# Optimization experiments

Hardware: AMD Instinct MI355X
Metric: run time of the kernel (lower is better)

## Reference

```python
import jax, jax.numpy as jnp
import numpy as np

B = 32768
D = 1024          # input_dim
SEL = 512         # select_dim (per-expert selected features)
E = 6             # num_experts
K = 3             # top_k
SH = 32           # shared_dim
INNER = 64        # cross-attn inner dim (4 heads * 16)
HID = 128         # expert hidden


def setup_inputs() -> dict:
    key = jax.random.key(0)
    ks = jax.random.split(key, 16)
    s = lambda i, shape, scale=0.02: (jax.random.normal(ks[i], shape, jnp.float32) * scale)
    return {
        "x": jax.random.normal(ks[0], (B, D), jnp.float32),
        # CrossAttention(query_dim=512, context_dim=512, heads=4, dim_head=16)
        "Wq": s(1, (512, INNER)),
        "Wk": s(2, (512, INNER)),
        "Wv": s(3, (512, INNER)),
        "Wo": s(4, (INNER, 512)),
        "bo": jnp.zeros((512,), jnp.float32),
        # shared_proj: Linear(512, 32)
        "Wsp": s(5, (512, SH)),
        "bsp": jnp.zeros((SH,), jnp.float32),
        # gate: Linear(1024, 6)
        "Wg": s(6, (D, E)),
        "bg": jnp.zeros((E,), jnp.float32),
        # per-expert feature-mask logits
        "mask_logits": jax.random.normal(ks[7], (E, D), jnp.float32),
        # expert MLPs: Linear(544,128) -> ReLU -> Linear(128,1), stacked over experts
        "W1": s(8, (E, SEL + SH, HID)),
        "b1": jnp.zeros((E, HID), jnp.float32),
        "W2": s(9, (E, HID, 1)),
        "b2": jnp.zeros((E, 1), jnp.float32),
    }


def _moe_forward(x, Wq, Wk, Wv, Wo, bo, Wsp, bsp, Wg, bg, mask_logits, W1, b1, W2, b2):
    x_sem = x[:, :512]
    x_vis = x[:, 512:]

    # CrossAttention with a single query token attending to a single context
    # token: softmax over one key is identically 1, so attn output == v.
    v = x_vis @ Wv                      # [B, INNER]
    shared_token = v @ Wo + bo          # to_out Linear, [B, 512]
    shared_info = shared_token @ Wsp + bsp  # [B, SH]

    # Gating: top-k experts per sample, softmax over selected logits
    gate_logits = x @ Wg + bg                       # [B, E]
    topk_scores, topk_idx = jax.lax.top_k(gate_logits, K)  # [B, K]
    topk_w = jax.nn.softmax(topk_scores, axis=1)    # [B, K]

    # Per-expert learned feature selection (top-512 of sigmoid(mask_logits));
    # sigmoid is monotonic but kept for faithfulness.
    mask_prob = jax.nn.sigmoid(mask_logits)         # [E, D]
    _, sel_idx = jax.lax.top_k(mask_prob, SEL)      # [E, SEL]

    # Dense expert evaluation (every expert on every sample), then gather the
    # routed outputs -- same math as the original scatter loop.
    x_sel = jnp.take(x, sel_idx, axis=1)            # [B, E, SEL]
    h = jnp.einsum('bes,esh->beh', x_sel, W1[:, :SEL, :])
    h = h + jnp.einsum('bd,edh->beh', shared_info, W1[:, SEL:, :])
    h = jax.nn.relu(h + b1[None])                   # [B, E, HID]
    expert_out = jnp.einsum('beh,eh->be', h, W2[:, :, 0]) + b2[None, :, 0]  # [B, E]

    routed = jnp.take_along_axis(expert_out, topk_idx, axis=1)  # [B, K]
    return jnp.sum(topk_w * routed, axis=1, keepdims=True)      # [B, 1]


def reference(x, Wq, Wk, Wv, Wo, bo, Wsp, bsp, Wg, bg, mask_logits, W1, b1, W2, b2):
    return _moe_forward(x, Wq, Wk, Wv, Wo, bo, Wsp, bsp, Wg, bg, mask_logits, W1, b1, W2, b2)
```

## Files before the change

### kernel.cpp

```cpp
#include <hip/hip_runtime.h>

#define B 32768
#define D 1024
#define SEL 512
#define E 6
#define K 3
#define SH 32
#define HID 128
#define NKT 16

typedef __attribute__((ext_vector_type(8))) short bf16x8;
typedef __attribute__((ext_vector_type(4))) float f32x4;

__device__ __forceinline__ unsigned short f2bf(float f) {
  unsigned u = __float_as_uint(f);
  return (unsigned short)((u + 0x7fffu + ((u >> 16) & 1u)) >> 16);
}
__device__ __forceinline__ float bf2f(unsigned short h) {
  return __uint_as_float((unsigned)h << 16);
}

__device__ __forceinline__ void gload_lds16(const void* g, void* l) {
  __builtin_amdgcn_global_load_lds(
      (const __attribute__((address_space(1))) void*)g,
      (__attribute__((address_space(3))) void*)l, 16, 0, 0);
}

__global__ void k_sel(const float* __restrict__ ml, int* __restrict__ inv,
                      int* __restrict__ cnt) {
  __shared__ float row[D];
  const int e = blockIdx.x, t = threadIdx.x;
  if (t == 0) cnt[e] = 0;
  row[t] = ml[e * D + t];
  __syncthreads();
  const float v = row[t];
  int rank = 0;
  for (int i = 0; i < D; ++i) {
    float u = row[i];
    rank += (u > v) || (u == v && i < t);
  }
  inv[e * D + t] = (rank < SEL) ? rank : -1;
}

__global__ __launch_bounds__(256) void k_wowsp(
    const float* __restrict__ Wo, const float* __restrict__ Wsp,
    const float* __restrict__ bo, const float* __restrict__ bsp,
    const float* __restrict__ Wg,
    float* __restrict__ WoWsp, float* __restrict__ bfull,
    unsigned short* __restrict__ WgS) {
  __shared__ float red[256];
  const int t = threadIdx.x;
  const int j = t & 31, chunk = t >> 5;
  const int blk = blockIdx.x;
  if (blk < 64) {
    const int i = blk;
    float p = 0.f;
    for (int c = chunk * 64; c < chunk * 64 + 64; ++c)
      p += Wo[i * 512 + c] * Wsp[c * SH + j];
    red[t] = p;
    __syncthreads();
    if (t < 32) {
      float s = 0.f;
      #pragma unroll
      for (int k = 0; k < 8; ++k) s += red[k * 32 + j];
      WoWsp[i * SH + j] = s;
    }
  } else if (blk == 64) {
    float p = 0.f;
    for (int c = chunk * 64; c < chunk * 64 + 64; ++c)
      p += bo[c] * Wsp[c * SH + j];
    red[t] = p;
    __syncthreads();
    if (t < 32) {
      float s = bsp[j];
      #pragma unroll
      for (int k = 0; k < 8; ++k) s += red[k * 32 + j];
      bfull[j] = s;
    }
  } else {
    const int idx = (blk - 65) * 256 + t;
    const int col = idx >> 10, k = idx & 1023;
    float wv = (col < E) ? Wg[(size_t)k * E + col] : 0.f;
    unsigned short hi = f2bf(wv);
    unsigned short lo = f2bf(wv - bf2f(hi));
    WgS[col * D + k] = hi;
    WgS[16 * D + col * D + k] = lo;
  }
}

__global__ __launch_bounds__(256) void k_wfull2(
    const float* __restrict__ Wv, const float* __restrict__ WoWsp,
    float* __restrict__ Wfull) {
  __shared__ float wsh[64 * SH];
  const int t = threadIdx.x;
  for (int idx = t; idx < 64 * SH; idx += 256) wsh[idx] = WoWsp[idx];
  __syncthreads();
  const int c = blockIdx.x * 8 + (t >> 5), j = t & 31;
  float p = 0.f;
  #pragma unroll 8
  for (int i = 0; i < 64; ++i) p += Wv[c * 64 + i] * wsh[i * SH + j];
  Wfull[c * SH + j] = p;
}

__global__ __launch_bounds__(256) void k_w1c(
    const float* __restrict__ W1, const float* __restrict__ b1,
    const int* __restrict__ inv, const float* __restrict__ Wfull,
    const float* __restrict__ bfull,
    unsigned short* __restrict__ W1eT, float* __restrict__ b1c) {
  __shared__ float w1b[SH];
  __shared__ float bf[SH];
  const int e = blockIdx.x >> 7, h = blockIdx.x & 127;
  const int t = threadIdx.x;
  const float* We = W1 + (size_t)e * (SEL + SH) * HID;
  if (t < SH) { w1b[t] = We[(size_t)(SEL + t) * HID + h]; bf[t] = bfull[t]; }
  __syncthreads();
  const int* iv = inv + e * D;
  unsigned short* dst = W1eT + ((size_t)e * HID + h) * D;
  #pragma unroll
  for (int it = 0; it < 4; ++it) {
    int d = t + it * 256;
    int s = iv[d];
    float v = (s >= 0) ? We[(size_t)s * HID + h] : 0.f;
    if (d >= 512) {
      const float* wf = Wfull + (size_t)(d - 512) * SH;
      float p = 0.f;
      #pragma unroll
      for (int j = 0; j < SH; ++j) p += wf[j] * w1b[j];
      v += p;
    }
    dst[d] = f2bf(v);
  }
  if (t == 0) {
    float p = b1[e * HID + h];
    for (int j = 0; j < SH; ++j) p += bf[j] * w1b[j];
    b1c[e * HID + h] = p;
  }
}

template<bool WRITE_XBF>
__global__ __launch_bounds__(256) void k_xgate(
    const float* __restrict__ x, const unsigned short* __restrict__ WgS,
    const float* __restrict__ Wg, const float* __restrict__ bg,
    unsigned short* __restrict__ xbf,
    int* __restrict__ cnt, int* __restrict__ clist, float* __restrict__ wlist) {
  __shared__ __align__(16) char ldsAh[64 * 128];
  __shared__ __align__(16) char ldsAl[64 * 128];
  __shared__ __align__(16) char ldsW[4096];
  __shared__ float gl_s[64][8];
  const int t = threadIdx.x;
  const int bm = blockIdx.x;
  const int w = t >> 6, lane = t & 63;
  const int g = lane >> 4, j = lane & 15;
  const int swz = ((lane & 7) * 16) ^ ((lane >> 3) << 4);

  const char* srcW = (const char*)WgS +
                     (size_t)(w * 8 + (lane >> 3)) * (D * 2) + swz;

  f32x4 acc = {0.f, 0.f, 0.f, 0.f};

  for (int kt = 0; kt < NKT; ++kt) {
    if (kt) __syncthreads();
    gload_lds16(srcW + kt * 128, ldsW + w * 1024);
    #pragma unroll
    for (int it = 0; it < 4; ++it) {
      int r = (t >> 4) + it * 16;
      const float4 v =
          *(const float4*)(x + (size_t)(bm * 64 + r) * D + kt * 64 + (t & 15) * 4);
      ushort4 hh, ll;
      hh.x = f2bf(v.x); hh.y = f2bf(v.y); hh.z = f2bf(v.z); hh.w = f2bf(v.w);
      ll.x = f2bf(v.x - bf2f(hh.x)); ll.y = f2bf(v.y - bf2f(hh.y));
      ll.z = f2bf(v.z - bf2f(hh.z)); ll.w = f2bf(v.w - bf2f(hh.w));
      if (WRITE_XBF)
        *(ushort4*)(xbf + (size_t)(bm * 64 + r) * D + kt * 64 + (t & 15) * 4) = hh;
      const int ao = r * 128 + (((t & 15) * 8) ^ ((r & 7) << 4));
      *(ushort4*)(ldsAh + ao) = hh;
      *(ushort4*)(ldsAl + ao) = ll;
    }
    __syncthreads();
    #pragma unroll
    for (int kk = 0; kk < 2; ++kk) {
      const int kb = kk * 64 + g * 16;
      const int wo = kb ^ ((j & 7) << 4);
      bf16x8 bh = *(const bf16x8*)(ldsW + j * 128 + wo);
      bf16x8 bl = *(const bf16x8*)(ldsW + 2048 + j * 128 + wo);
      const int row = w * 16 + j;
      const int aoff = row * 128 + (kb ^ ((row & 7) << 4));
      bf16x8 ah = *(const bf16x8*)(ldsAh + aoff);
      bf16x8 al = *(const bf16x8*)(ldsAl + aoff);
      acc = __builtin_amdgcn_mfma_f32_16x16x32_bf16(ah, bh, acc, 0, 0, 0);
      acc = __builtin_amdgcn_mfma_f32_16x16x32_bf16(ah, bl, acc, 0, 0, 0);
      acc = __builtin_amdgcn_mfma_f32_16x16x32_bf16(al, bh, acc, 0, 0, 0);
      acc = __builtin_amdgcn_mfma_f32_16x16x32_bf16(al, bl, acc, 0, 0, 0);
    }
  }
  if (j < E) {
    #pragma unroll
    for (int ri = 0; ri < 4; ++ri)
      gl_s[w * 16 + g * 4 + ri][j] = acc[ri];
  }
  __syncthreads();
  if (t < 64) {
    const int tok = bm * 64 + t;
    float gv[E];
    #pragma unroll
    for (int e2 = 0; e2 < E; ++e2) gv[e2] = gl_s[t][e2] + bg[e2];

    float s4[4];
    {
      bool used[E] = {};
      #pragma unroll
      for (int k = 0; k < 4; ++k) {
        float best = -1e30f; int bi = 0;
        for (int e2 = 0; e2 < E; ++e2)
          if (!used[e2] && gv[e2] > best) { best = gv[e2]; bi = e2; }
        used[bi] = true; s4[k] = best;
      }
    }
    unsigned long long flags = __ballot(s4[2] - s4[3] < 4e-3f);
    while (flags) {
      const int fl = __ffsll((long long)flags) - 1;
      flags &= flags - 1;
      const int tokf = bm * 64 + fl;
      float ex[E] = {};
      for (int i = 0; i < 16; ++i) {
        const int d = t + 64 * i;
        float xv = x[(size_t)tokf * D + d];
        const float* wr = Wg + (size_t)d * E;
        #pragma unroll
        for (int e2 = 0; e2 < E; ++e2) ex[e2] += xv * wr[e2];
      }
      #pragma unroll
      for (int e2 = 0; e2 < E; ++e2) {
        float s = ex[e2];
        s += __shfl_xor(s, 1); s += __shfl_xor(s, 2); s += __shfl_xor(s, 4);
        s += __shfl_xor(s, 8); s += __shfl_xor(s, 16); s += __shfl_xor(s, 32);
        ex[e2] = s;
      }
      if (t == fl) {
        #pragma unroll
        for (int e2 = 0; e2 < E; ++e2) gv[e2] = ex[e2] + bg[e2];
      }
    }
    int idx[K]; float sc[K];
    bool used[E] = {};
    #pragma unroll
    for (int k = 0; k < K; ++k) {
      float best = -1e30f; int bi = 0;
      for (int e2 = 0; e2 < E; ++e2)
        if (!used[e2] && gv[e2] > best) { best = gv[e2]; bi = e2; }
      used[bi] = true; sc[k] = best; idx[k] = bi;
    }
    float s1 = __expf(sc[1] - sc[0]), s2 = __expf(sc[2] - sc[0]);
    float inv_s = 1.f / (1.f + s1 + s2);
    float tw[K] = {inv_s, s1 * inv_s, s2 * inv_s};
    const unsigned long long below = (1ULL << t) - 1ULL;
    #pragma unroll
    for (int e2 = 0; e2 < E; ++e2) {
      int myk = -1;
      #pragma unroll
      for (int k = 0; k < K; ++k) if (idx[k] == e2) myk = k;
      unsigned long long m = __ballot(myk >= 0);
      if (m) {
        int tot = __popcll(m);
        int leader = __ffsll((long long)m) - 1;
        int base = 0;
        if (t == leader) base = atomicAdd(&cnt[e2], tot);
        base = __shfl(base, leader);
        if (myk >= 0) {
          int pos = base + __popcll(m & below);
          clist[e2 * B + pos] = (tok << 2) | myk;
          wlist[e2 * B + pos] = tw[myk];
        }
      }
    }
  }
}

template<int AMODE>
__global__ __launch_bounds__(256) void k_gemm(
    const float* __restrict__ x, const unsigned short* __restrict__ xbf,
    const unsigned short* __restrict__ W1eT,
    const int* __restrict__ cnt, const int* __restrict__ clist,
    const float* __restrict__ wlist,
    const float* __restrict__ b1c, const float* __restrict__ W2,
    const float* __restrict__ b2, float* __restrict__ eo4) {
  __shared__ __align__(16) char ldsA[128 * 128];
  __shared__ __align__(16) char ldsB[128 * 128];
  __shared__ int tokl[128];
  __shared__ float red[128];

  const int t = threadIdx.x;
  const int e = blockIdx.x >> 8;
  const int bm = blockIdx.x & 255;
  const int n = cnt[e];
  if (bm * 128 >= n) return;
  const int cb = e * B;

  if (t < 128) {
    int gr = bm * 128 + t;
    tokl[t] = clist[cb + (gr < n ? gr : 0)] >> 2;
  }
  __syncthreads();

  const int w = t >> 6, lane = t & 63;
  const int g = lane >> 4, j = lane & 15;
  const int swz = ((lane & 7) * 16) ^ ((lane >> 3) << 4);

  const char* srcB[4];
  #pragma unroll
  for (int q = 0; q < 4; ++q)
    srcB[q] = (const char*)W1eT +
              (size_t)(e * HID + w * 32 + q * 8 + (lane >> 3)) * (D * 2) + swz;
  const char* srcA[4];
  if (AMODE == 0) {
    #pragma unroll
    for (int q = 0; q < 4; ++q)
      srcA[q] = (const char*)xbf +
                (size_t)tokl[w * 32 + q * 8 + (lane >> 3)] * 2048 + swz;
  }

  f32x4 acc[2][8] = {};

  for (int kt = 0; kt < NKT; ++kt) {
    if (kt) __syncthreads();
    if (AMODE == 0) {
      #pragma unroll
      for (int q = 0; q < 4; ++q)
        gload_lds16(srcA[q] + kt * 128, ldsA + w * 4096 + q * 1024);
    }
    #pragma unroll
    for (int q = 0; q < 4; ++q)
      gload_lds16(srcB[q] + kt * 128, ldsB + w * 4096 + q * 1024);
    if (AMODE == 1) {
      #pragma unroll
      for (int it = 0; it < 8; ++it) {
        int r = (t >> 4) + it * 16;
        const float4 v =
            *(const float4*)(x + (size_t)tokl[r] * D + kt * 64 + (t & 15) * 4);
        ushort4 h4;
        h4.x = f2bf(v.x); h4.y = f2bf(v.y); h4.z = f2bf(v.z); h4.w = f2bf(v.w);
        *(ushort4*)(ldsA + r * 128 + (((t & 15) * 8) ^ ((r & 7) << 4))) = h4;
      }
    }
    __syncthreads();
    #pragma unroll
    for (int kk = 0; kk < 2; ++kk) {
      const int kb = kk * 64 + g * 16;
      bf16x8 aF[2];
      #pragma unroll
      for (int fm = 0; fm < 2; ++fm) {
        int row = w * 32 + fm * 16 + j;
        aF[fm] = *(const bf16x8*)(ldsA + row * 128 + (kb ^ ((row & 7) << 4)));
      }
      #pragma unroll
      for (int fn = 0; fn < 8; ++fn) {
        int col = fn * 16 + j;
        bf16x8 bF = *(const bf16x8*)(ldsB + col * 128 + (kb ^ ((col & 7) << 4)));
        acc[0][fn] = __builtin_amdgcn_mfma_f32_16x16x32_bf16(aF[0], bF, acc[0][fn], 0, 0, 0);
        acc[1][fn] = __builtin_amdgcn_mfma_f32_16x16x32_bf16(aF[1], bF, acc[1][fn], 0, 0, 0);
      }
    }
  }

  float vb1[8], vw2[8];
  #pragma unroll
  for (int fn = 0; fn < 8; ++fn) {
    int col = fn * 16 + j;
    vb1[fn] = b1c[e * HID + col];
    vw2[fn] = W2[e * HID + col];
  }
  #pragma unroll
  for (int fm = 0; fm < 2; ++fm) {
    #pragma unroll
    for (int r = 0; r < 4; ++r) {
      float s = 0.f;
      #pragma unroll
      for (int fn = 0; fn < 8; ++fn)
        s += fmaxf(acc[fm][fn][r] + vb1[fn], 0.f) * vw2[fn];
      s += __shfl_xor(s, 1); s += __shfl_xor(s, 2);
      s += __shfl_xor(s, 4); s += __shfl_xor(s, 8);
      if (j == 0) red[w * 32 + fm * 16 + g * 4 + r] = s;
    }
  }
  __syncthreads();
  if (t < 128) {
    int gr = bm * 128 + t;
    if (gr < n) {
      int en = clist[cb + gr];
      eo4[(size_t)(en >> 2) * 4 + (en & 3)] = wlist[cb + gr] * (red[t] + b2[e]);
    }
  }
}

__global__ void k_comb2(const float* __restrict__ eo4, float* __restrict__ out) {
  const int tok = blockIdx.x * 256 + threadIdx.x;
  float4 v = *(const float4*)(eo4 + (size_t)tok * 4);
  out[tok] = v.x + v.y + v.z;
}

extern "C" void kernel_launch(void* const* d_in, const int* in_sizes, int n_in,
                              void* d_out, int out_size, void* d_ws, size_t ws_size,
                              hipStream_t stream) {
  const float* x   = (const float*)d_in[0];
  const float* Wv  = (const float*)d_in[3];
  const float* Wo  = (const float*)d_in[4];
  const float* bo  = (const float*)d_in[5];
  const float* Wsp = (const float*)d_in[6];
  const float* bsp = (const float*)d_in[7];
  const float* Wg  = (const float*)d_in[8];
  const float* bg  = (const float*)d_in[9];
  const float* ml  = (const float*)d_in[10];
  const float* W1  = (const float*)d_in[11];
  const float* b1  = (const float*)d_in[12];
  const float* W2  = (const float*)d_in[13];
  const float* b2  = (const float*)d_in[14];
  float* out = (float*)d_out;

  char* ws = (char*)d_ws;
  int*   inv   = (int*)ws;
  float* WoWsp = (float*)(ws + 32768);
  float* Wfull = (float*)(ws + 49152);
  float* bfull = (float*)(ws + 114688);
  float* b1c   = (float*)(ws + 118784);
  int*   cnt   = (int*)(ws + 126976);
  unsigned short* WgS = (unsigned short*)(ws + 131072);
  int*   clist = (int*)(ws + 262144);
  float* wlist = (float*)(ws + 1048576);
  float* eo4   = (float*)(ws + 1835008);
  unsigned short* W1eT = (unsigned short*)(ws + 2359296);
  unsigned short* xbf  = (unsigned short*)(ws + 3932160);
  const bool use_xbf = ws_size >= (size_t)3932160 + (size_t)B * D * 2;

  k_sel<<<E, D, 0, stream>>>(ml, inv, cnt);
  k_wowsp<<<129, 256, 0, stream>>>(Wo, Wsp, bo, bsp, Wg, WoWsp, bfull, WgS);
  k_wfull2<<<64, 256, 0, stream>>>(Wv, WoWsp, Wfull);
  k_w1c<<<E * HID, 256, 0, stream>>>(W1, b1, inv, Wfull, bfull, W1eT, b1c);
  if (use_xbf)
    k_xgate<true><<<B / 64, 256, 0, stream>>>(x, WgS, Wg, bg, xbf, cnt, clist, wlist);
  else
    k_xgate<false><<<B / 64, 256, 0, stream>>>(x, WgS, Wg, bg, xbf, cnt, clist, wlist);
  if (use_xbf)
    k_gemm<0><<<E * 256, 256, 0, stream>>>(x, xbf, W1eT, cnt, clist, wlist, b1c, W2, b2, eo4);
  else
    k_gemm<1><<<E * 256, 256, 0, stream>>>(x, xbf, W1eT, cnt, clist, wlist, b1c, W2, b2, eo4);
  k_comb2<<<B / 256, 256, 0, stream>>>(eo4, out);
}
```

Baseline: 175.7 us.

## Split gate GEMM K across waves and drop per-tile block barriers

```diff
diff --git a/kernel.cpp b/kernel.cpp
--- a/kernel.cpp
+++ b/kernel.cpp
@@ -143,67 +143,79 @@
     const float* __restrict__ Wg, const float* __restrict__ bg,
     unsigned short* __restrict__ xbf,
     int* __restrict__ cnt, int* __restrict__ clist, float* __restrict__ wlist) {
-  __shared__ __align__(16) char ldsAh[64 * 128];
-  __shared__ __align__(16) char ldsAl[64 * 128];
-  __shared__ __align__(16) char ldsW[4096];
-  __shared__ float gl_s[64][8];
+  __shared__ __align__(16) char ldsAh[4][32 * 128];
+  __shared__ __align__(16) char ldsAl[4][32 * 128];
+  __shared__ float gl_s[4][32][8];
   const int t = threadIdx.x;
   const int bm = blockIdx.x;
-  const int w = t >> 6, lane = t & 63;
-  const int g = lane >> 4, j = lane & 15;
-  const int swz = ((lane & 7) * 16) ^ ((lane >> 3) << 4);
-
-  const char* srcW = (const char*)WgS +
-                     (size_t)(w * 8 + (lane >> 3)) * (D * 2) + swz;
-
-  f32x4 acc = {0.f, 0.f, 0.f, 0.f};
-
-  for (int kt = 0; kt < NKT; ++kt) {
-    if (kt) __syncthreads();
-    gload_lds16(srcW + kt * 128, ldsW + w * 1024);
-    #pragma unroll
-    for (int it = 0; it < 4; ++it) {
-      int r = (t >> 4) + it * 16;
-      const float4 v =
-          *(const float4*)(x + (size_t)(bm * 64 + r) * D + kt * 64 + (t & 15) * 4);
+  const int w = t >> 6, l = t & 63;
+  const int g = l >> 4, j = l & 15;
+  const int tok0 = bm * 32;
+  const int k0 = w * 256;
+
+  char* Ah = ldsAh[w];
+  char* Al = ldsAl[w];
+
+  f32x4 acc0 = {0.f, 0.f, 0.f, 0.f};
+  f32x4 acc1 = {0.f, 0.f, 0.f, 0.f};
+
+  #pragma unroll
+  for (int tile = 0; tile < 4; ++tile) {
+    const int kb = k0 + tile * 64;
+    #pragma unroll
+    for (int i = 0; i < 8; ++i) {
+      const int r = (l >> 4) + i * 4;
+      const int c = l & 15;
+      float4 v = *(const float4*)(x + (size_t)(tok0 + r) * D + kb + c * 4);
       ushort4 hh, ll;
       hh.x = f2bf(v.x); hh.y = f2bf(v.y); hh.z = f2bf(v.z); hh.w = f2bf(v.w);
       ll.x = f2bf(v.x - bf2f(hh.x)); ll.y = f2bf(v.y - bf2f(hh.y));
       ll.z = f2bf(v.z - bf2f(hh.z)); ll.w = f2bf(v.w - bf2f(hh.w));
       if (WRITE_XBF)
-        *(ushort4*)(xbf + (size_t)(bm * 64 + r) * D + kt * 64 + (t & 15) * 4) = hh;
-      const int ao = r * 128 + (((t & 15) * 8) ^ ((r & 7) << 4));
-      *(ushort4*)(ldsAh + ao) = hh;
-      *(ushort4*)(ldsAl + ao) = ll;
-    }
-    __syncthreads();
+        *(ushort4*)(xbf + (size_t)(tok0 + r) * D + kb + c * 4) = hh;
+      const int ao = r * 128 + ((c * 8) ^ ((r & 7) << 4));
+      *(ushort4*)(Ah + ao) = hh;
+      *(ushort4*)(Al + ao) = ll;
+    }
     #pragma unroll
     for (int kk = 0; kk < 2; ++kk) {
-      const int kb = kk * 64 + g * 16;
-      const int wo = kb ^ ((j & 7) << 4);
-      bf16x8 bh = *(const bf16x8*)(ldsW + j * 128 + wo);
-      bf16x8 bl = *(const bf16x8*)(ldsW + 2048 + j * 128 + wo);
-      const int row = w * 16 + j;
-      const int aoff = row * 128 + (kb ^ ((row & 7) << 4));
-      bf16x8 ah = *(const bf16x8*)(ldsAh + aoff);
-      bf16x8 al = *(const bf16x8*)(ldsAl + aoff);
-      acc = __builtin_amdgcn_mfma_f32_16x16x32_bf16(ah, bh, acc, 0, 0, 0);
-      acc = __builtin_amdgcn_mfma_f32_16x16x32_bf16(ah, bl, acc, 0, 0, 0);
-      acc = __builtin_amdgcn_mfma_f32_16x16x32_bf16(al, bh, acc, 0, 0, 0);
-      acc = __builtin_amdgcn_mfma_f32_16x16x32_bf16(al, bl, acc, 0, 0, 0);
+      bf16x8 bh = *(const bf16x8*)(WgS + (size_t)j * D + kb + kk * 32 + g * 8);
+      bf16x8 bl = *(const bf16x8*)(WgS + (size_t)(16 + j) * D + kb + kk * 32 + g * 8);
+      #pragma unroll
+      for (int rf = 0; rf < 2; ++rf) {
+        const int row = rf * 16 + j;
+        const int aoff = row * 128 + ((kk * 64 + g * 16) ^ ((row & 7) << 4));
+        bf16x8 ah = *(const bf16x8*)(Ah + aoff);
+        bf16x8 al = *(const bf16x8*)(Al + aoff);
+        if (rf == 0) {
+          acc0 = __builtin_amdgcn_mfma_f32_16x16x32_bf16(ah, bh, acc0, 0, 0, 0);
+          acc0 = __builtin_amdgcn_mfma_f32_16x16x32_bf16(ah, bl, acc0, 0, 0, 0);
+          acc0 = __builtin_amdgcn_mfma_f32_16x16x32_bf16(al, bh, acc0, 0, 0, 0);
+          acc0 = __builtin_amdgcn_mfma_f32_16x16x32_bf16(al, bl, acc0, 0, 0, 0);
+        } else {
+          acc1 = __builtin_amdgcn_mfma_f32_16x16x32_bf16(ah, bh, acc1, 0, 0, 0);
+          acc1 = __builtin_amdgcn_mfma_f32_16x16x32_bf16(ah, bl, acc1, 0, 0, 0);
+          acc1 = __builtin_amdgcn_mfma_f32_16x16x32_bf16(al, bh, acc1, 0, 0, 0);
+          acc1 = __builtin_amdgcn_mfma_f32_16x16x32_bf16(al, bl, acc1, 0, 0, 0);
+        }
+      }
     }
   }
   if (j < E) {
     #pragma unroll
-    for (int ri = 0; ri < 4; ++ri)
-      gl_s[w * 16 + g * 4 + ri][j] = acc[ri];
-  }
-  __syncthreads();
-  if (t < 64) {
-    const int tok = bm * 64 + t;
+    for (int ri = 0; ri < 4; ++ri) {
+      gl_s[w][g * 4 + ri][j] = acc0[ri];
+      gl_s[w][16 + g * 4 + ri][j] = acc1[ri];
+    }
+  }
+  __syncthreads();
+  if (t < 32) {
+    const int tok = tok0 + t;
     float gv[E];
     #pragma unroll
-    for (int e2 = 0; e2 < E; ++e2) gv[e2] = gl_s[t][e2] + bg[e2];
+    for (int e2 = 0; e2 < E; ++e2)
+      gv[e2] = gl_s[0][t][e2] + gl_s[1][t][e2] + gl_s[2][t][e2] +
+               gl_s[3][t][e2] + bg[e2];
 
     float s4[4];
     {
@@ -220,10 +232,10 @@
     while (flags) {
       const int fl = __ffsll((long long)flags) - 1;
       flags &= flags - 1;
-      const int tokf = bm * 64 + fl;
+      const int tokf = tok0 + fl;
       float ex[E] = {};
-      for (int i = 0; i < 16; ++i) {
-        const int d = t + 64 * i;
+      for (int i = 0; i < 32; ++i) {
+        const int d = t + 32 * i;
         float xv = x[(size_t)tokf * D + d];
         const float* wr = Wg + (size_t)d * E;
         #pragma unroll
@@ -233,7 +245,7 @@
       for (int e2 = 0; e2 < E; ++e2) {
         float s = ex[e2];
         s += __shfl_xor(s, 1); s += __shfl_xor(s, 2); s += __shfl_xor(s, 4);
-        s += __shfl_xor(s, 8); s += __shfl_xor(s, 16); s += __shfl_xor(s, 32);
+        s += __shfl_xor(s, 8); s += __shfl_xor(s, 16);
         ex[e2] = s;
       }
       if (t == fl) {
@@ -436,9 +448,9 @@
   k_wfull2<<<64, 256, 0, stream>>>(Wv, WoWsp, Wfull);
   k_w1c<<<E * HID, 256, 0, stream>>>(W1, b1, inv, Wfull, bfull, W1eT, b1c);
   if (use_xbf)
-    k_xgate<true><<<B / 64, 256, 0, stream>>>(x, WgS, Wg, bg, xbf, cnt, clist, wlist);
+    k_xgate<true><<<B / 32, 256, 0, stream>>>(x, WgS, Wg, bg, xbf, cnt, clist, wlist);
   else
-    k_xgate<false><<<B / 64, 256, 0, stream>>>(x, WgS, Wg, bg, xbf, cnt, clist, wlist);
+    k_xgate<false><<<B / 32, 256, 0, stream>>>(x, WgS, Wg, bg, xbf, cnt, clist, wlist);
   if (use_xbf)
     k_gemm<0><<<E * 256, 256, 0, stream>>>(x, xbf, W1eT, cnt, clist, wlist, b1c, W2, b2, eo4);
   else
```

Measured after the change: 214.5 us. 1.22x slower.

## Shrink gate kernel tile to 16 tokens and split bf16 MFMA terms across waves

Applied to the files above, without the earlier changes.

```diff
diff --git a/kernel.cpp b/kernel.cpp
--- a/kernel.cpp
+++ b/kernel.cpp
@@ -143,15 +143,17 @@
     const float* __restrict__ Wg, const float* __restrict__ bg,
     unsigned short* __restrict__ xbf,
     int* __restrict__ cnt, int* __restrict__ clist, float* __restrict__ wlist) {
-  __shared__ __align__(16) char ldsAh[64 * 128];
-  __shared__ __align__(16) char ldsAl[64 * 128];
+  __shared__ __align__(16) char ldsAh[16 * 128];
+  __shared__ __align__(16) char ldsAl[16 * 128];
   __shared__ __align__(16) char ldsW[4096];
-  __shared__ float gl_s[64][8];
+  __shared__ float gl_s[4][16][8];
   const int t = threadIdx.x;
   const int bm = blockIdx.x;
   const int w = t >> 6, lane = t & 63;
   const int g = lane >> 4, j = lane & 15;
+  const int tok0 = bm * 16;
   const int swz = ((lane & 7) * 16) ^ ((lane >> 3) << 4);
+  const int r0 = t >> 4, c = t & 15;
 
   const char* srcW = (const char*)WgS +
                      (size_t)(w * 8 + (lane >> 3)) * (D * 2) + swz;
@@ -159,20 +161,17 @@
   f32x4 acc = {0.f, 0.f, 0.f, 0.f};
 
   for (int kt = 0; kt < NKT; ++kt) {
-    if (kt) __syncthreads();
     gload_lds16(srcW + kt * 128, ldsW + w * 1024);
-    #pragma unroll
-    for (int it = 0; it < 4; ++it) {
-      int r = (t >> 4) + it * 16;
+    {
       const float4 v =
-          *(const float4*)(x + (size_t)(bm * 64 + r) * D + kt * 64 + (t & 15) * 4);
+          *(const float4*)(x + (size_t)(tok0 + r0) * D + kt * 64 + c * 4);
       ushort4 hh, ll;
       hh.x = f2bf(v.x); hh.y = f2bf(v.y); hh.z = f2bf(v.z); hh.w = f2bf(v.w);
       ll.x = f2bf(v.x - bf2f(hh.x)); ll.y = f2bf(v.y - bf2f(hh.y));
       ll.z = f2bf(v.z - bf2f(hh.z)); ll.w = f2bf(v.w - bf2f(hh.w));
       if (WRITE_XBF)
-        *(ushort4*)(xbf + (size_t)(bm * 64 + r) * D + kt * 64 + (t & 15) * 4) = hh;
-      const int ao = r * 128 + (((t & 15) * 8) ^ ((r & 7) << 4));
+        *(ushort4*)(xbf + (size_t)(tok0 + r0) * D + kt * 64 + c * 4) = hh;
+      const int ao = r0 * 128 + ((c * 8) ^ ((r0 & 7) << 4));
       *(ushort4*)(ldsAh + ao) = hh;
       *(ushort4*)(ldsAl + ao) = ll;
     }
@@ -181,29 +180,38 @@
     for (int kk = 0; kk < 2; ++kk) {
       const int kb = kk * 64 + g * 16;
       const int wo = kb ^ ((j & 7) << 4);
-      bf16x8 bh = *(const bf16x8*)(ldsW + j * 128 + wo);
-      bf16x8 bl = *(const bf16x8*)(ldsW + 2048 + j * 128 + wo);
-      const int row = w * 16 + j;
-      const int aoff = row * 128 + (kb ^ ((row & 7) << 4));
-      bf16x8 ah = *(const bf16x8*)(ldsAh + aoff);
-      bf16x8 al = *(const bf16x8*)(ldsAl + aoff);
-      acc = __builtin_amdgcn_mfma_f32_16x16x32_bf16(ah, bh, acc, 0, 0, 0);
-      acc = __builtin_amdgcn_mfma_f32_16x16x32_bf16(ah, bl, acc, 0, 0, 0);
-      acc = __builtin_amdgcn_mfma_f32_16x16x32_bf16(al, bh, acc, 0, 0, 0);
-      acc = __builtin_amdgcn_mfma_f32_16x16x32_bf16(al, bl, acc, 0, 0, 0);
-    }
+      const int aoff = j * 128 + (kb ^ ((j & 7) << 4));
+      bf16x8 aF, bF;
+      if (w == 0) {
+        aF = *(const bf16x8*)(ldsAh + aoff);
+        bF = *(const bf16x8*)(ldsW + j * 128 + wo);
+      } else if (w == 1) {
+        aF = *(const bf16x8*)(ldsAl + aoff);
+        bF = *(const bf16x8*)(ldsW + 2048 + j * 128 + wo);
+      } else if (w == 2) {
+        aF = *(const bf16x8*)(ldsAh + aoff);
+        bF = *(const bf16x8*)(ldsW + 2048 + j * 128 + wo);
+      } else {
+        aF = *(const bf16x8*)(ldsAl + aoff);
+        bF = *(const bf16x8*)(ldsW + j * 128 + wo);
+      }
+      acc = __builtin_amdgcn_mfma_f32_16x16x32_bf16(aF, bF, acc, 0, 0, 0);
+    }
+    __syncthreads();
   }
   if (j < E) {
     #pragma unroll
     for (int ri = 0; ri < 4; ++ri)
-      gl_s[w * 16 + g * 4 + ri][j] = acc[ri];
-  }
-  __syncthreads();
-  if (t < 64) {
-    const int tok = bm * 64 + t;
+      gl_s[w][g * 4 + ri][j] = acc[ri];
+  }
+  __syncthreads();
+  if (t < 16) {
+    const int tok = tok0 + t;
     float gv[E];
     #pragma unroll
-    for (int e2 = 0; e2 < E; ++e2) gv[e2] = gl_s[t][e2] + bg[e2];
+    for (int e2 = 0; e2 < E; ++e2)
+      gv[e2] = gl_s[0][t][e2] + gl_s[1][t][e2] + gl_s[2][t][e2] +
+               gl_s[3][t][e2] + bg[e2];
 
     float s4[4];
     {
@@ -220,10 +228,10 @@
     while (flags) {
       const int fl = __ffsll((long long)flags) - 1;
       flags &= flags - 1;
-      const int tokf = bm * 64 + fl;
+      const int tokf = tok0 + fl;
       float ex[E] = {};
-      for (int i = 0; i < 16; ++i) {
-        const int d = t + 64 * i;
+      for (int i = 0; i < 64; ++i) {
+        const int d = t + 16 * i;
         float xv = x[(size_t)tokf * D + d];
         const float* wr = Wg + (size_t)d * E;
         #pragma unroll
@@ -232,8 +240,8 @@
       #pragma unroll
       for (int e2 = 0; e2 < E; ++e2) {
         float s = ex[e2];
-        s += __shfl_xor(s, 1); s += __shfl_xor(s, 2); s += __shfl_xor(s, 4);
-        s += __shfl_xor(s, 8); s += __shfl_xor(s, 16); s += __shfl_xor(s, 32);
+        s += __shfl_xor(s, 1); s += __shfl_xor(s, 2);
+        s += __shfl_xor(s, 4); s += __shfl_xor(s, 8);
         ex[e2] = s;
       }
       if (t == fl) {
@@ -436,9 +444,9 @@
   k_wfull2<<<64, 256, 0, stream>>>(Wv, WoWsp, Wfull);
   k_w1c<<<E * HID, 256, 0, stream>>>(W1, b1, inv, Wfull, bfull, W1eT, b1c);
   if (use_xbf)
-    k_xgate<true><<<B / 64, 256, 0, stream>>>(x, WgS, Wg, bg, xbf, cnt, clist, wlist);
+    k_xgate<true><<<B / 16, 256, 0, stream>>>(x, WgS, Wg, bg, xbf, cnt, clist, wlist);
   else
-    k_xgate<false><<<B / 64, 256, 0, stream>>>(x, WgS, Wg, bg, xbf, cnt, clist, wlist);
+    k_xgate<false><<<B / 16, 256, 0, stream>>>(x, WgS, Wg, bg, xbf, cnt, clist, wlist);
   if (use_xbf)
     k_gemm<0><<<E * 256, 256, 0, stream>>>(x, xbf, W1eT, cnt, clist, wlist, b1c, W2, b2, eo4);
   else
```

Result: slower. 282.8 us (+60.9%).

## Split gate GEMM over K into 4 blocks and move top-k to separate kernel

Applied to the files above, without the earlier changes.

```diff
diff --git a/kernel.cpp b/kernel.cpp
--- a/kernel.cpp
+++ b/kernel.cpp
@@ -140,17 +140,16 @@
 template<bool WRITE_XBF>
 __global__ __launch_bounds__(256) void k_xgate(
     const float* __restrict__ x, const unsigned short* __restrict__ WgS,
-    const float* __restrict__ Wg, const float* __restrict__ bg,
-    unsigned short* __restrict__ xbf,
-    int* __restrict__ cnt, int* __restrict__ clist, float* __restrict__ wlist) {
+    unsigned short* __restrict__ xbf, float* __restrict__ gpart) {
   __shared__ __align__(16) char ldsAh[64 * 128];
   __shared__ __align__(16) char ldsAl[64 * 128];
   __shared__ __align__(16) char ldsW[4096];
-  __shared__ float gl_s[64][8];
   const int t = threadIdx.x;
-  const int bm = blockIdx.x;
+  const int bm = blockIdx.x >> 2;
+  const int ks = blockIdx.x & 3;
   const int w = t >> 6, lane = t & 63;
   const int g = lane >> 4, j = lane & 15;
+  const int tok0 = bm * 64;
   const int swz = ((lane & 7) * 16) ^ ((lane >> 3) << 4);
 
   const char* srcW = (const char*)WgS +
@@ -158,20 +157,21 @@
 
   f32x4 acc = {0.f, 0.f, 0.f, 0.f};
 
-  for (int kt = 0; kt < NKT; ++kt) {
-    if (kt) __syncthreads();
+  for (int i = 0; i < 4; ++i) {
+    const int kt = ks * 4 + i;
+    if (i) __syncthreads();
     gload_lds16(srcW + kt * 128, ldsW + w * 1024);
     #pragma unroll
     for (int it = 0; it < 4; ++it) {
       int r = (t >> 4) + it * 16;
       const float4 v =
-          *(const float4*)(x + (size_t)(bm * 64 + r) * D + kt * 64 + (t & 15) * 4);
+          *(const float4*)(x + (size_t)(tok0 + r) * D + kt * 64 + (t & 15) * 4);
       ushort4 hh, ll;
       hh.x = f2bf(v.x); hh.y = f2bf(v.y); hh.z = f2bf(v.z); hh.w = f2bf(v.w);
       ll.x = f2bf(v.x - bf2f(hh.x)); ll.y = f2bf(v.y - bf2f(hh.y));
       ll.z = f2bf(v.z - bf2f(hh.z)); ll.w = f2bf(v.w - bf2f(hh.w));
       if (WRITE_XBF)
-        *(ushort4*)(xbf + (size_t)(bm * 64 + r) * D + kt * 64 + (t & 15) * 4) = hh;
+        *(ushort4*)(xbf + (size_t)(tok0 + r) * D + kt * 64 + (t & 15) * 4) = hh;
       const int ao = r * 128 + (((t & 15) * 8) ^ ((r & 7) << 4));
       *(ushort4*)(ldsAh + ao) = hh;
       *(ushort4*)(ldsAl + ao) = ll;
@@ -196,81 +196,90 @@
   if (j < E) {
     #pragma unroll
     for (int ri = 0; ri < 4; ++ri)
-      gl_s[w * 16 + g * 4 + ri][j] = acc[ri];
-  }
-  __syncthreads();
-  if (t < 64) {
-    const int tok = bm * 64 + t;
-    float gv[E];
-    #pragma unroll
-    for (int e2 = 0; e2 < E; ++e2) gv[e2] = gl_s[t][e2] + bg[e2];
-
-    float s4[4];
-    {
-      bool used[E] = {};
-      #pragma unroll
-      for (int k = 0; k < 4; ++k) {
-        float best = -1e30f; int bi = 0;
-        for (int e2 = 0; e2 < E; ++e2)
-          if (!used[e2] && gv[e2] > best) { best = gv[e2]; bi = e2; }
-        used[bi] = true; s4[k] = best;
-      }
-    }
-    unsigned long long flags = __ballot(s4[2] - s4[3] < 4e-3f);
-    while (flags) {
-      const int fl = __ffsll((long long)flags) - 1;
-      flags &= flags - 1;
-      const int tokf = bm * 64 + fl;
-      float ex[E] = {};
-      for (int i = 0; i < 16; ++i) {
-        const int d = t + 64 * i;
-        float xv = x[(size_t)tokf * D + d];
-        const float* wr = Wg + (size_t)d * E;
-        #pragma unroll
-        for (int e2 = 0; e2 < E; ++e2) ex[e2] += xv * wr[e2];
-      }
-      #pragma unroll
-      for (int e2 = 0; e2 < E; ++e2) {
-        float s = ex[e2];
-        s += __shfl_xor(s, 1); s += __shfl_xor(s, 2); s += __shfl_xor(s, 4);
-        s += __shfl_xor(s, 8); s += __shfl_xor(s, 16); s += __shfl_xor(s, 32);
-        ex[e2] = s;
-      }
-      if (t == fl) {
-        #pragma unroll
-        for (int e2 = 0; e2 < E; ++e2) gv[e2] = ex[e2] + bg[e2];
-      }
-    }
-    int idx[K]; float sc[K];
+      gpart[(size_t)(tok0 + w * 16 + g * 4 + ri) * 32 + ks * 8 + j] = acc[ri];
+  }
+}
+
+__global__ __launch_bounds__(256) void k_gtopk(
+    const float* __restrict__ gpart, const float* __restrict__ x,
+    const float* __restrict__ Wg, const float* __restrict__ bg,
+    int* __restrict__ cnt, int* __restrict__ clist, float* __restrict__ wlist) {
+  const int tok = blockIdx.x * 256 + threadIdx.x;
+  const int l = threadIdx.x & 63;
+  const int wtok0 = tok - l;
+  float gv[E];
+  #pragma unroll
+  for (int e2 = 0; e2 < E; ++e2) {
+    float s = bg[e2];
+    #pragma unroll
+    for (int ks = 0; ks < 4; ++ks) s += gpart[(size_t)tok * 32 + ks * 8 + e2];
+    gv[e2] = s;
+  }
+  float s4[4];
+  {
     bool used[E] = {};
     #pragma unroll
-    for (int k = 0; k < K; ++k) {
+    for (int k = 0; k < 4; ++k) {
       float best = -1e30f; int bi = 0;
       for (int e2 = 0; e2 < E; ++e2)
         if (!used[e2] && gv[e2] > best) { best = gv[e2]; bi = e2; }
-      used[bi] = true; sc[k] = best; idx[k] = bi;
-    }
-    float s1 = __expf(sc[1] - sc[0]), s2 = __expf(sc[2] - sc[0]);
-    float inv_s = 1.f / (1.f + s1 + s2);
-    float tw[K] = {inv_s, s1 * inv_s, s2 * inv_s};
-    const unsigned long long below = (1ULL << t) - 1ULL;
+      used[bi] = true; s4[k] = best;
+    }
+  }
+  unsigned long long flags = __ballot(s4[2] - s4[3] < 4e-3f);
+  while (flags) {
+    const int fl = __ffsll((long long)flags) - 1;
+    flags &= flags - 1;
+    const int tokf = wtok0 + fl;
+    float ex[E] = {};
+    for (int i = 0; i < 16; ++i) {
+      const int d = l + 64 * i;
+      float xv = x[(size_t)tokf * D + d];
+      const float* wr = Wg + (size_t)d * E;
+      #pragma unroll
+      for (int e2 = 0; e2 < E; ++e2) ex[e2] += xv * wr[e2];
+    }
     #pragma unroll
     for (int e2 = 0; e2 < E; ++e2) {
-      int myk = -1;
-      #pragma unroll
-      for (int k = 0; k < K; ++k) if (idx[k] == e2) myk = k;
-      unsigned long long m = __ballot(myk >= 0);
-      if (m) {
-        int tot = __popcll(m);
-        int leader = __ffsll((long long)m) - 1;
-        int base = 0;
-        if (t == leader) base = atomicAdd(&cnt[e2], tot);
-        base = __shfl(base, leader);
-        if (myk >= 0) {
-          int pos = base + __popcll(m & below);
-          clist[e2 * B + pos] = (tok << 2) | myk;
-          wlist[e2 * B + pos] = tw[myk];
-        }
+      float s = ex[e2];
+      s += __shfl_xor(s, 1); s += __shfl_xor(s, 2); s += __shfl_xor(s, 4);
+      s += __shfl_xor(s, 8); s += __shfl_xor(s, 16); s += __shfl_xor(s, 32);
+      ex[e2] = s;
+    }
+    if (l == fl) {
+      #pragma unroll
+      for (int e2 = 0; e2 < E; ++e2) gv[e2] = ex[e2] + bg[e2];
+    }
+  }
+  int idx[K]; float sc[K];
+  bool used[E] = {};
+  #pragma unroll
+  for (int k = 0; k < K; ++k) {
+    float best = -1e30f; int bi = 0;
+    for (int e2 = 0; e2 < E; ++e2)
+      if (!used[e2] && gv[e2] > best) { best = gv[e2]; bi = e2; }
+    used[bi] = true; sc[k] = best; idx[k] = bi;
+  }
+  float s1 = __expf(sc[1] - sc[0]), s2 = __expf(sc[2] - sc[0]);
+  float inv_s = 1.f / (1.f + s1 + s2);
+  float tw[K] = {inv_s, s1 * inv_s, s2 * inv_s};
+  const unsigned long long below = (1ULL << l) - 1ULL;
+  #pragma unroll
+  for (int e2 = 0; e2 < E; ++e2) {
+    int myk = -1;
+    #pragma unroll
+    for (int k = 0; k < K; ++k) if (idx[k] == e2) myk = k;
+    unsigned long long m = __ballot(myk >= 0);
+    if (m) {
+      int tot = __popcll(m);
+      int leader = __ffsll((long long)m) - 1;
+      int base = 0;
+      if (l == leader) base = atomicAdd(&cnt[e2], tot);
+      base = __shfl(base, leader);
+      if (myk >= 0) {
+        int pos = base + __popcll(m & below);
+        clist[e2 * B + pos] = (tok << 2) | myk;
+        wlist[e2 * B + pos] = tw[myk];
       }
     }
   }
@@ -428,17 +437,19 @@
   float* wlist = (float*)(ws + 1048576);
   float* eo4   = (float*)(ws + 1835008);
   unsigned short* W1eT = (unsigned short*)(ws + 2359296);
-  unsigned short* xbf  = (unsigned short*)(ws + 3932160);
-  const bool use_xbf = ws_size >= (size_t)3932160 + (size_t)B * D * 2;
+  float* gpart = (float*)(ws + 3932160);
+  unsigned short* xbf  = (unsigned short*)(ws + 8126464);
+  const bool use_xbf = ws_size >= (size_t)8126464 + (size_t)B * D * 2;
 
   k_sel<<<E, D, 0, stream>>>(ml, inv, cnt);
   k_wowsp<<<129, 256, 0, stream>>>(Wo, Wsp, bo, bsp, Wg, WoWsp, bfull, WgS);
   k_wfull2<<<64, 256, 0, stream>>>(Wv, WoWsp, Wfull);
   k_w1c<<<E * HID, 256, 0, stream>>>(W1, b1, inv, Wfull, bfull, W1eT, b1c);
   if (use_xbf)
-    k_xgate<true><<<B / 64, 256, 0, stream>>>(x, WgS, Wg, bg, xbf, cnt, clist, wlist);
+    k_xgate<true><<<(B / 64) * 4, 256, 0, stream>>>(x, WgS, xbf, gpart);
   else
-    k_xgate<false><<<B / 64, 256, 0, stream>>>(x, WgS, Wg, bg, xbf, cnt, clist, wlist);
+    k_xgate<false><<<(B / 64) * 4, 256, 0, stream>>>(x, WgS, xbf, gpart);
+  k_gtopk<<<B / 256, 256, 0, stream>>>(gpart, x, Wg, bg, cnt, clist, wlist);
   if (use_xbf)
     k_gemm<0><<<E * 256, 256, 0, stream>>>(x, xbf, W1eT, cnt, clist, wlist, b1c, W2, b2, eo4);
   else
```

Result: slower. 184.4 us (+4.9%).
